# Kernel tuning notes

Measured on AMD Instinct MI355X. Metric: run time of the kernel, lower is better.

The kernel has to match this reference:

```python
import jax, jax.numpy as jnp
import numpy as np

N = 50000      # nodes
E = 600000     # edges
D_IN = 128
D_H = 128
D_OUT = 64


def setup_inputs() -> dict:
    key = jax.random.key(0)
    ks = jax.random.split(key, 10)
    x = jax.random.normal(ks[0], (N, D_IN), dtype=jnp.float32)
    edge_index = jax.random.randint(ks[1], (2, E), 0, N, dtype=jnp.int32)
    def lin(k, fan_out, fan_in):
        s = 1.0 / np.sqrt(fan_in)
        return jax.random.uniform(k, (fan_out, fan_in), jnp.float32, -s, s)
    W0 = lin(ks[2], D_H, D_IN);   b0 = jnp.zeros((D_H,), jnp.float32)
    W1 = lin(ks[3], D_H, D_H);    b1 = jnp.zeros((D_H,), jnp.float32)
    W2 = lin(ks[4], D_H, D_H);    b2 = jnp.zeros((D_H,), jnp.float32)
    W3 = lin(ks[5], D_OUT, D_H);  b3 = jnp.zeros((D_OUT,), jnp.float32)
    return {"x": x, "edge_index": edge_index,
            "W0": W0, "b0": b0, "W1": W1, "b1": b1,
            "W2": W2, "b2": b2, "W3": W3, "b3": b3}


def reference(x, edge_index, W0, b0, W1, b1, W2, b2, W3, b3):
    n = x.shape[0]
    loops = jnp.arange(n, dtype=edge_index.dtype)
    row = jnp.concatenate([edge_index[0], loops])  # sources (with self-loops)
    col = jnp.concatenate([edge_index[1], loops])  # targets
    # symmetric normalization D^-1/2 (A+I) D^-1/2 (PyG GCNConv default)
    deg = jax.ops.segment_sum(jnp.ones(row.shape, x.dtype), col, num_segments=n)
    dinv = jnp.where(deg > 0, jax.lax.rsqrt(deg), 0.0)
    norm = dinv[row] * dinv[col]  # [E+N]

    def gcn_conv(h, W, b):
        h = h @ W.T                              # [n, out]
        msg = h[row] * norm[:, None]             # gather + scale
        out = jax.ops.segment_sum(msg, col, num_segments=n)  # scatter-add
        return out + b

    h = jax.nn.relu(gcn_conv(x, W0, b0))   # Dropout is identity in eval mode
    h = jax.nn.relu(gcn_conv(h, W1, b1))
    h = jax.nn.relu(gcn_conv(h, W2, b2))
    return gcn_conv(h, W3, b3)
```

## Files before the change

kernel.cpp:

```cpp
#include <hip/hip_runtime.h>

#define D_INF 128
#define D_HF  128
#define D_OUTF 64

typedef __attribute__((ext_vector_type(8))) short bf16x8;
typedef __attribute__((ext_vector_type(4))) float f32x4;
typedef unsigned short u16;
typedef unsigned int   u32;

__device__ inline u16 f2bf(float f) {
    u32 u = __float_as_uint(f);
    u32 r = (u + 0x7fffu + ((u >> 16) & 1u)) >> 16;
    return (u16)r;
}
__device__ inline float bf2f(u16 h) { return __uint_as_float(((u32)h) << 16); }

__global__ void k_zero_i32(int* p, int n) {
    int i = blockIdx.x * blockDim.x + threadIdx.x;
    if (i < n) p[i] = 0;
}

__global__ void k_count(const int* __restrict__ colv, int* __restrict__ cnt, int E) {
    int e = blockIdx.x * blockDim.x + threadIdx.x;
    if (e < E) atomicAdd(&cnt[colv[e]], 1);
}

__global__ void k_scan_block(int* __restrict__ cnt, int* __restrict__ rp,
                             int* __restrict__ bsum, float* __restrict__ dinv, int n) {
    __shared__ int sm[256];
    int t = threadIdx.x;
    int i = blockIdx.x * 256 + t;
    int v = (i < n) ? cnt[i] : 0;
    sm[t] = v;
    __syncthreads();
    for (int off = 1; off < 256; off <<= 1) {
        int x = sm[t];
        int y = (t >= off) ? sm[t - off] : 0;
        __syncthreads();
        sm[t] = x + y;
        __syncthreads();
    }
    if (i < n) {
        rp[i] = sm[t] - v;
        dinv[i] = (float)(1.0 / sqrt((double)(v + 1)));
        cnt[i] = 0;
    }
    if (t == 255) bsum[blockIdx.x] = sm[t];
}

__global__ void k_scan_bsum(int* __restrict__ bsum, int nb) {
    __shared__ int sm[256];
    int t = threadIdx.x;
    int v = (t < nb) ? bsum[t] : 0;
    sm[t] = v;
    __syncthreads();
    for (int off = 1; off < 256; off <<= 1) {
        int x = sm[t];
        int y = (t >= off) ? sm[t - off] : 0;
        __syncthreads();
        sm[t] = x + y;
        __syncthreads();
    }
    if (t < nb) bsum[t] = sm[t] - v;
}

__global__ void k_scan_add2(int* __restrict__ rp, const int* __restrict__ bsum, int n) {
    int i = blockIdx.x * 256 + threadIdx.x;
    if (i < n) rp[i] += bsum[blockIdx.x];
}

__global__ void k_scatter(const int* __restrict__ row, const int* __restrict__ colv,
                          const float* __restrict__ dinv, const int* __restrict__ rp,
                          int* __restrict__ fill, int* __restrict__ csr_src,
                          float* __restrict__ csr_w, int E) {
    int e = blockIdx.x * blockDim.x + threadIdx.x;
    if (e >= E) return;
    int r = row[e], c = colv[e];
    int pos = rp[c] + atomicAdd(&fill[c], 1);
    csr_src[pos] = r;
    csr_w[pos] = dinv[r] * dinv[c];
}

__global__ void k_split_x(const float* __restrict__ x, u16* __restrict__ Xcat,
                          int Nreal, int Mpad) {
    int idx = blockIdx.x * 256 + threadIdx.x;
    int total = Mpad * 32;
    if (idx >= total) return;
    const int row = idx >> 5, c4 = (idx & 31) * 4;
    float4 v = make_float4(0.f, 0.f, 0.f, 0.f);
    if (row < Nreal) v = *(const float4*)(x + (size_t)row * 128 + c4);
    u16 h0 = f2bf(v.x), h1 = f2bf(v.y), h2 = f2bf(v.z), h3 = f2bf(v.w);
    u16 l0 = f2bf(v.x - bf2f(h0)), l1 = f2bf(v.y - bf2f(h1));
    u16 l2 = f2bf(v.z - bf2f(h2)), l3 = f2bf(v.w - bf2f(h3));
    u16* dst = Xcat + (size_t)row * 256 + c4;
    *(u32*)(dst)       = (u32)h0 | ((u32)h1 << 16);
    *(u32*)(dst + 2)   = (u32)h2 | ((u32)h3 << 16);
    *(u32*)(dst + 128) = (u32)l0 | ((u32)l1 << 16);
    *(u32*)(dst + 130) = (u32)l2 | ((u32)l3 << 16);
}

__global__ void k_split_w(const float* __restrict__ W0, const float* __restrict__ W1,
                          const float* __restrict__ W2, const float* __restrict__ W3,
                          u16* __restrict__ Wcat) {
    const int l = blockIdx.y;
    const float* W = (l == 0) ? W0 : (l == 1) ? W1 : (l == 2) ? W2 : W3;
    const int rows = (l == 3) ? 64 : 128;
    int idx = blockIdx.x * 256 + threadIdx.x;
    if (idx >= rows * 128) return;
    const int r = idx >> 7, c = idx & 127;
    float v = W[idx];
    u16 h = f2bf(v);
    u16 lo = f2bf(v - bf2f(h));
    u16* dst = Wcat + (size_t)l * 128 * 256 + (size_t)r * 256 + c;
    dst[0]   = h;
    dst[128] = lo;
}

template <int FM>
__global__ __launch_bounds__(256)
void k_gemm_mfma(const u16* __restrict__ Xcat, const u16* __restrict__ Wcat,
                 float* __restrict__ H) {
    constexpr int Dout = (FM == 4) ? 128 : 64;
    const int tid = threadIdx.x;
    const int wave = tid >> 6, lane = tid & 63;
    const int wm = (FM == 4) ? (wave >> 1) : wave;
    const int wn = (FM == 4) ? (wave & 1) : 0;
    const int row_base = blockIdx.x * 128 + wm * (FM * 16);
    const int col_base = wn * 64;
    const int lr = lane & 15;
    const int kg = lane >> 4;

    f32x4 acc[FM][4] = {};

    #pragma unroll 2
    for (int ks = 0; ks < 8; ++ks) {
        const int k0 = ks * 32 + kg * 8;
        bf16x8 a[FM], b[4];
        #pragma unroll
        for (int i = 0; i < FM; ++i)
            a[i] = *(const bf16x8*)(Xcat + (size_t)(row_base + i * 16 + lr) * 256 + k0);
        #pragma unroll
        for (int j = 0; j < 4; ++j)
            b[j] = *(const bf16x8*)(Wcat + (size_t)(col_base + j * 16 + lr) * 256 + k0);
        #pragma unroll
        for (int i = 0; i < FM; ++i)
            #pragma unroll
            for (int j = 0; j < 4; ++j)
                acc[i][j] = __builtin_amdgcn_mfma_f32_16x16x32_bf16(a[i], b[j], acc[i][j], 0, 0, 0);
    }

    #pragma unroll
    for (int i = 0; i < FM; ++i) {
        const int r0 = row_base + i * 16 + kg * 4;
        #pragma unroll
        for (int j = 0; j < 4; ++j) {
            const int c = col_base + j * 16 + lr;
            #pragma unroll
            for (int q = 0; q < 4; ++q)
                H[(size_t)(r0 + q) * Dout + c] = acc[i][j][q];
        }
    }
}

template <int D, int OUT_MODE>
__global__ void k_agg_gather(const float* __restrict__ H, const float* __restrict__ dinv,
                             const int* __restrict__ rp, const int* __restrict__ csr_src,
                             const float* __restrict__ csr_w, const float* __restrict__ b,
                             void* __restrict__ out, int N, int E) {
    const int node = blockIdx.x * 4 + (threadIdx.x >> 6);
    const int lane = threadIdx.x & 63;
    if (node >= N) return;
    const int beg = rp[node];
    const int end = (node == N - 1) ? E : rp[node + 1];
    const int deg = end - beg;
    const float di = dinv[node];
    const double wself = (double)di * (double)di;

    if (D == 128) {
        const int d0 = lane * 2;
        double a0[8] = {}, a1[8] = {};
        {
            const float2 hs = *(const float2*)(H + (size_t)node * D + d0);
            a0[0] = wself * hs.x; a1[0] = wself * hs.y;
        }
        for (int base = 0; base < deg; base += 64) {
            const int m = min(64, deg - base);
            int s_l = 0; float w_l = 0.f;
            if (lane < m) {
                s_l = csr_src[beg + base + lane];
                w_l = csr_w[beg + base + lane];
            }
            const int m16 = (m + 15) & ~15;
            for (int j = 0; j < m16; j += 16) {
                int s[16]; float w[16];
                #pragma unroll
                for (int q = 0; q < 16; ++q) {
                    s[q] = __shfl(s_l, j + q);
                    w[q] = __shfl(w_l, j + q);
                }
                float2 h[16];
                #pragma unroll
                for (int q = 0; q < 16; ++q)
                    h[q] = *(const float2*)(H + (size_t)s[q] * D + d0);
                #pragma unroll
                for (int q = 0; q < 16; ++q) {
                    a0[q & 7] += (double)w[q] * h[q].x;
                    a1[q & 7] += (double)w[q] * h[q].y;
                }
            }
        }
        double A0 = ((a0[0] + a0[1]) + (a0[2] + a0[3])) + ((a0[4] + a0[5]) + (a0[6] + a0[7]));
        double A1 = ((a1[0] + a1[1]) + (a1[2] + a1[3])) + ((a1[4] + a1[5]) + (a1[6] + a1[7]));
        float v0 = (float)(A0 + (double)b[d0]);
        float v1 = (float)(A1 + (double)b[d0 + 1]);
        if (OUT_MODE == 1) {
            v0 = fmaxf(v0, 0.0f); v1 = fmaxf(v1, 0.0f);
            const u16 h0 = f2bf(v0), h1 = f2bf(v1);
            const u16 l0 = f2bf(v0 - bf2f(h0)), l1 = f2bf(v1 - bf2f(h1));
            u16* xc = (u16*)out + (size_t)node * 256 + d0;
            *(u32*)(xc)       = (u32)h0 | ((u32)h1 << 16);
            *(u32*)(xc + 128) = (u32)l0 | ((u32)l1 << 16);
        } else {
            *(float2*)((float*)out + (size_t)node * D + d0) = make_float2(v0, v1);
        }
    } else {
        const int half = lane >> 5;
        const int l32 = lane & 31;
        const int d0 = l32 * 2;
        double a0[8] = {}, a1[8] = {};
        if (half == 0) {
            const float2 hs = *(const float2*)(H + (size_t)node * D + d0);
            a0[0] = wself * hs.x; a1[0] = wself * hs.y;
        }
        for (int base = 0; base < deg; base += 64) {
            const int m = min(64, deg - base);
            int s_l = 0; float w_l = 0.f;
            if (lane < m) {
                s_l = csr_src[beg + base + lane];
                w_l = csr_w[beg + base + lane];
            }
            const int m16 = (m + 15) & ~15;
            for (int j = 0; j < m16; j += 16) {
                int s[8]; float w[8];
                #pragma unroll
                for (int q = 0; q < 8; ++q) {
                    const int e = j + 2 * q + half;
                    s[q] = __shfl(s_l, e);
                    w[q] = __shfl(w_l, e);
                }
                float2 h[8];
                #pragma unroll
                for (int q = 0; q < 8; ++q)
                    h[q] = *(const float2*)(H + (size_t)s[q] * D + d0);
                #pragma unroll
                for (int q = 0; q < 8; ++q) {
                    a0[q] += (double)w[q] * h[q].x;
                    a1[q] += (double)w[q] * h[q].y;
                }
            }
        }
        double A0 = ((a0[0] + a0[1]) + (a0[2] + a0[3])) + ((a0[4] + a0[5]) + (a0[6] + a0[7]));
        double A1 = ((a1[0] + a1[1]) + (a1[2] + a1[3])) + ((a1[4] + a1[5]) + (a1[6] + a1[7]));
        A0 += __shfl_xor(A0, 32);
        A1 += __shfl_xor(A1, 32);
        if (half == 0) {
            float v0 = (float)(A0 + (double)b[d0]);
            float v1 = (float)(A1 + (double)b[d0 + 1]);
            *(float2*)((float*)out + (size_t)node * D + d0) = make_float2(v0, v1);
        }
    }
}

extern "C" void kernel_launch(void* const* d_in, const int* in_sizes, int n_in,
                              void* d_out, int out_size, void* d_ws, size_t ws_size,
                              hipStream_t stream) {
    const float* x  = (const float*)d_in[0];
    const int*   ei = (const int*)d_in[1];
    const float* W[4] = {(const float*)d_in[2], (const float*)d_in[4],
                         (const float*)d_in[6], (const float*)d_in[8]};
    const float* B[4] = {(const float*)d_in[3], (const float*)d_in[5],
                         (const float*)d_in[7], (const float*)d_in[9]};
    const int N = in_sizes[0] / D_INF;
    const int E = in_sizes[1] / 2;
    const int Mpad = (N + 127) & ~127;
    const int* row  = ei;
    const int* colv = ei + E;

    size_t nPad = ((size_t)N + 255) & ~(size_t)255;
    size_t ePad = ((size_t)E + 255) & ~(size_t)255;
    float* dinv    = (float*)d_ws;
    int*   cnt     = (int*)(dinv + nPad);
    int*   bsum    = cnt + nPad;
    int*   rp      = bsum + 256;
    int*   csr_src = rp + nPad;
    float* csr_w   = (float*)(csr_src + ePad);
    float* Hbuf    = csr_w + ePad;
    u16*   Xcat    = (u16*)(Hbuf + (size_t)Mpad * 128);
    u16*   Wcat    = Xcat + (size_t)Mpad * 256;

    const int TB = 256;
    int nbN = (N + TB - 1) / TB;
    int nbE = (E + TB - 1) / TB;

    k_zero_i32<<<nbN, TB, 0, stream>>>(cnt, N);
    k_count<<<nbE, TB, 0, stream>>>(colv, cnt, E);
    k_scan_block<<<nbN, TB, 0, stream>>>(cnt, rp, bsum, dinv, N);
    k_scan_bsum<<<1, 256, 0, stream>>>(bsum, nbN);
    k_scan_add2<<<nbN, TB, 0, stream>>>(rp, bsum, N);
    k_scatter<<<nbE, TB, 0, stream>>>(row, colv, dinv, rp, cnt, csr_src, csr_w, E);

    k_split_x<<<(Mpad * 32 + TB - 1) / TB, TB, 0, stream>>>(x, Xcat, N, Mpad);
    {
        dim3 g(64, 4);
        k_split_w<<<g, TB, 0, stream>>>(W[0], W[1], W[2], W[3], Wcat);
    }

    const int aggGrid = (N + 3) / 4;
    const int gemmGrid = Mpad / 128;

    for (int l = 0; l < 3; ++l) {
        k_gemm_mfma<4><<<gemmGrid, 256, 0, stream>>>(Xcat, Wcat + (size_t)l * 128 * 256, Hbuf);
        k_agg_gather<128, 1><<<aggGrid, TB, 0, stream>>>(Hbuf, dinv, rp, csr_src, csr_w,
                                                         B[l], (void*)Xcat, N, E);
    }
    k_gemm_mfma<2><<<gemmGrid, 256, 0, stream>>>(Xcat, Wcat + (size_t)3 * 128 * 256, Hbuf);
    k_agg_gather<64, 0><<<aggGrid, TB, 0, stream>>>(Hbuf, dinv, rp, csr_src, csr_w,
                                                    B[3], d_out, N, E);
}
```

Baseline: 331.9 us.

## Bucket CSR edges by source-node quartile and gather per phase

Builds the CSR with four sub-buckets per destination node, keyed by which quarter of the node range the source falls in. Each aggregation walks the buckets in order, so the gathers tend to stay within a narrower address range. The edge-batch unroll drops from 16 to 8, which cuts padding waste on low-degree nodes. In exchange, the prefix scan covers four times as many entries, there is an extra degree kernel, and the per-phase loop adds overhead with less memory-level parallelism per batch.

```diff
diff --git a/kernel.cpp b/kernel.cpp
--- a/kernel.cpp
+++ b/kernel.cpp
@@ -3,6 +3,7 @@
 #define D_INF 128
 #define D_HF  128
 #define D_OUTF 64
+#define NPH 4
 
 typedef __attribute__((ext_vector_type(8))) short bf16x8;
 typedef __attribute__((ext_vector_type(4))) float f32x4;
@@ -21,13 +22,23 @@
     if (i < n) p[i] = 0;
 }
 
-__global__ void k_count(const int* __restrict__ colv, int* __restrict__ cnt, int E) {
+__global__ void k_count4(const int* __restrict__ rowv, const int* __restrict__ colv,
+                         int* __restrict__ cnt4, int E, int q4) {
     int e = blockIdx.x * blockDim.x + threadIdx.x;
-    if (e < E) atomicAdd(&cnt[colv[e]], 1);
+    if (e >= E) return;
+    int ph = min(NPH - 1, rowv[e] / q4);
+    atomicAdd(&cnt4[colv[e] * NPH + ph], 1);
+}
+
+__global__ void k_dinv4(const int* __restrict__ cnt4, float* __restrict__ dinv, int n) {
+    int i = blockIdx.x * blockDim.x + threadIdx.x;
+    if (i >= n) return;
+    int deg = cnt4[i * NPH] + cnt4[i * NPH + 1] + cnt4[i * NPH + 2] + cnt4[i * NPH + 3] + 1;
+    dinv[i] = (float)(1.0 / sqrt((double)deg));
 }
 
 __global__ void k_scan_block(int* __restrict__ cnt, int* __restrict__ rp,
-                             int* __restrict__ bsum, float* __restrict__ dinv, int n) {
+                             int* __restrict__ bsum, int n) {
     __shared__ int sm[256];
     int t = threadIdx.x;
     int i = blockIdx.x * 256 + t;
@@ -43,19 +54,18 @@
     }
     if (i < n) {
         rp[i] = sm[t] - v;
-        dinv[i] = (float)(1.0 / sqrt((double)(v + 1)));
         cnt[i] = 0;
     }
     if (t == 255) bsum[blockIdx.x] = sm[t];
 }
 
 __global__ void k_scan_bsum(int* __restrict__ bsum, int nb) {
-    __shared__ int sm[256];
+    __shared__ int sm[1024];
     int t = threadIdx.x;
     int v = (t < nb) ? bsum[t] : 0;
     sm[t] = v;
     __syncthreads();
-    for (int off = 1; off < 256; off <<= 1) {
+    for (int off = 1; off < 1024; off <<= 1) {
         int x = sm[t];
         int y = (t >= off) ? sm[t - off] : 0;
         __syncthreads();
@@ -70,14 +80,16 @@
     if (i < n) rp[i] += bsum[blockIdx.x];
 }
 
-__global__ void k_scatter(const int* __restrict__ row, const int* __restrict__ colv,
-                          const float* __restrict__ dinv, const int* __restrict__ rp,
+__global__ void k_scatter(const int* __restrict__ rowv, const int* __restrict__ colv,
+                          const float* __restrict__ dinv, const int* __restrict__ rpp,
                           int* __restrict__ fill, int* __restrict__ csr_src,
-                          float* __restrict__ csr_w, int E) {
+                          float* __restrict__ csr_w, int E, int q4) {
     int e = blockIdx.x * blockDim.x + threadIdx.x;
     if (e >= E) return;
-    int r = row[e], c = colv[e];
-    int pos = rp[c] + atomicAdd(&fill[c], 1);
+    int r = rowv[e], c = colv[e];
+    int ph = min(NPH - 1, r / q4);
+    int slot = c * NPH + ph;
+    int pos = rpp[slot] + atomicAdd(&fill[slot], 1);
     csr_src[pos] = r;
     csr_w[pos] = dinv[r] * dinv[c];
 }
@@ -165,17 +177,15 @@
 
 template <int D, int OUT_MODE>
 __global__ void k_agg_gather(const float* __restrict__ H, const float* __restrict__ dinv,
-                             const int* __restrict__ rp, const int* __restrict__ csr_src,
+                             const int* __restrict__ rpp, const int* __restrict__ csr_src,
                              const float* __restrict__ csr_w, const float* __restrict__ b,
                              void* __restrict__ out, int N, int E) {
     const int node = blockIdx.x * 4 + (threadIdx.x >> 6);
     const int lane = threadIdx.x & 63;
     if (node >= N) return;
-    const int beg = rp[node];
-    const int end = (node == N - 1) ? E : rp[node + 1];
-    const int deg = end - beg;
     const float di = dinv[node];
     const double wself = (double)di * (double)di;
+    const int* rpn = rpp + NPH * node;
 
     if (D == 128) {
         const int d0 = lane * 2;
@@ -184,29 +194,35 @@
             const float2 hs = *(const float2*)(H + (size_t)node * D + d0);
             a0[0] = wself * hs.x; a1[0] = wself * hs.y;
         }
-        for (int base = 0; base < deg; base += 64) {
-            const int m = min(64, deg - base);
-            int s_l = 0; float w_l = 0.f;
-            if (lane < m) {
-                s_l = csr_src[beg + base + lane];
-                w_l = csr_w[beg + base + lane];
-            }
-            const int m16 = (m + 15) & ~15;
-            for (int j = 0; j < m16; j += 16) {
-                int s[16]; float w[16];
-                #pragma unroll
-                for (int q = 0; q < 16; ++q) {
-                    s[q] = __shfl(s_l, j + q);
-                    w[q] = __shfl(w_l, j + q);
+        #pragma unroll
+        for (int ph = 0; ph < NPH; ++ph) {
+            const int pbeg = rpn[ph];
+            const int pend = (node == N - 1 && ph == NPH - 1) ? E : rpn[ph + 1];
+            const int pdeg = pend - pbeg;
+            for (int base = 0; base < pdeg; base += 64) {
+                const int m = min(64, pdeg - base);
+                int s_l = 0; float w_l = 0.f;
+                if (lane < m) {
+                    s_l = csr_src[pbeg + base + lane];
+                    w_l = csr_w[pbeg + base + lane];
                 }
-                float2 h[16];
-                #pragma unroll
-                for (int q = 0; q < 16; ++q)
-                    h[q] = *(const float2*)(H + (size_t)s[q] * D + d0);
-                #pragma unroll
-                for (int q = 0; q < 16; ++q) {
-                    a0[q & 7] += (double)w[q] * h[q].x;
-                    a1[q & 7] += (double)w[q] * h[q].y;
+                const int m8 = (m + 7) & ~7;
+                for (int j = 0; j < m8; j += 8) {
+                    int s[8]; float w[8];
+                    #pragma unroll
+                    for (int q = 0; q < 8; ++q) {
+                        s[q] = __shfl(s_l, j + q);
+                        w[q] = __shfl(w_l, j + q);
+                    }
+                    float2 h[8];
+                    #pragma unroll
+                    for (int q = 0; q < 8; ++q)
+                        h[q] = *(const float2*)(H + (size_t)s[q] * D + d0);
+                    #pragma unroll
+                    for (int q = 0; q < 8; ++q) {
+                        a0[q] += (double)w[q] * h[q].x;
+                        a1[q] += (double)w[q] * h[q].y;
+                    }
                 }
             }
         }
@@ -228,40 +244,46 @@
         const int half = lane >> 5;
         const int l32 = lane & 31;
         const int d0 = l32 * 2;
-        double a0[8] = {}, a1[8] = {};
+        double a0[4] = {}, a1[4] = {};
         if (half == 0) {
             const float2 hs = *(const float2*)(H + (size_t)node * D + d0);
             a0[0] = wself * hs.x; a1[0] = wself * hs.y;
         }
-        for (int base = 0; base < deg; base += 64) {
-            const int m = min(64, deg - base);
-            int s_l = 0; float w_l = 0.f;
-            if (lane < m) {
-                s_l = csr_src[beg + base + lane];
-                w_l = csr_w[beg + base + lane];
-            }
-            const int m16 = (m + 15) & ~15;
-            for (int j = 0; j < m16; j += 16) {
-                int s[8]; float w[8];
-                #pragma unroll
-                for (int q = 0; q < 8; ++q) {
-                    const int e = j + 2 * q + half;
-                    s[q] = __shfl(s_l, e);
-                    w[q] = __shfl(w_l, e);
+        #pragma unroll
+        for (int ph = 0; ph < NPH; ++ph) {
+            const int pbeg = rpn[ph];
+            const int pend = (node == N - 1 && ph == NPH - 1) ? E : rpn[ph + 1];
+            const int pdeg = pend - pbeg;
+            for (int base = 0; base < pdeg; base += 64) {
+                const int m = min(64, pdeg - base);
+                int s_l = 0; float w_l = 0.f;
+                if (lane < m) {
+                    s_l = csr_src[pbeg + base + lane];
+                    w_l = csr_w[pbeg + base + lane];
                 }
-                float2 h[8];
-                #pragma unroll
-                for (int q = 0; q < 8; ++q)
-                    h[q] = *(const float2*)(H + (size_t)s[q] * D + d0);
-                #pragma unroll
-                for (int q = 0; q < 8; ++q) {
-                    a0[q] += (double)w[q] * h[q].x;
-                    a1[q] += (double)w[q] * h[q].y;
+                const int m8 = (m + 7) & ~7;
+                for (int j = 0; j < m8; j += 8) {
+                    int s[4]; float w[4];
+                    #pragma unroll
+                    for (int q = 0; q < 4; ++q) {
+                        const int e = j + 2 * q + half;
+                        s[q] = __shfl(s_l, e);
+                        w[q] = __shfl(w_l, e);
+                    }
+                    float2 h[4];
+                    #pragma unroll
+                    for (int q = 0; q < 4; ++q)
+                        h[q] = *(const float2*)(H + (size_t)s[q] * D + d0);
+                    #pragma unroll
+                    for (int q = 0; q < 4; ++q) {
+                        a0[q] += (double)w[q] * h[q].x;
+                        a1[q] += (double)w[q] * h[q].y;
+                    }
                 }
             }
         }
-        double A0 = ((a0[0] + a0[1]) + (a0[2] + a0[3])) + ((a0[4] + a0[5]) + (a0[6] + a0[7]));
-        double A1 = ((a1[0] + a1[1]) + (a1[2] + a1[3])) + ((a1[4] + a1[5]) + (a1[6] + a1[7]));
+        double A0 = (a0[0] + a0[1]) + (a0[2] + a0[3]);
+        double A1 = (a1[0] + a1[1]) + (a1[2] + a1[3]);
         A0 += __shfl_xor(A0, 32);
         A1 += __shfl_xor(A1, 32);
         if (half == 0) {
@@ -284,31 +306,36 @@
     const int N = in_sizes[0] / D_INF;
     const int E = in_sizes[1] / 2;
     const int Mpad = (N + 127) & ~127;
-    const int* row  = ei;
+    const int* rowv = ei;
     const int* colv = ei + E;
-
-    size_t nPad = ((size_t)N + 255) & ~(size_t)255;
-    size_t ePad = ((size_t)E + 255) & ~(size_t)255;
+    const int N4 = N * NPH;
+    const int q4 = (N + NPH - 1) / NPH;
+
+    size_t nPad  = ((size_t)N + 255) & ~(size_t)255;
+    size_t n4Pad = ((size_t)N4 + 255) & ~(size_t)255;
+    size_t ePad  = ((size_t)E + 255) & ~(size_t)255;
     float* dinv    = (float*)d_ws;
-    int*   cnt     = (int*)(dinv + nPad);
-    int*   bsum    = cnt + nPad;
-    int*   rp      = bsum + 256;
-    int*   csr_src = rp + nPad;
+    int*   cnt4    = (int*)(dinv + nPad);
+    int*   bsum    = cnt4 + n4Pad;
+    int*   rpp     = bsum + 1024;
+    int*   csr_src = rpp + n4Pad;
     float* csr_w   = (float*)(csr_src + ePad);
     float* Hbuf    = csr_w + ePad;
     u16*   Xcat    = (u16*)(Hbuf + (size_t)Mpad * 128);
     u16*   Wcat    = Xcat + (size_t)Mpad * 256;
 
     const int TB = 256;
-    int nbN = (N + TB - 1) / TB;
-    int nbE = (E + TB - 1) / TB;
-
-    k_zero_i32<<<nbN, TB, 0, stream>>>(cnt, N);
-    k_count<<<nbE, TB, 0, stream>>>(colv, cnt, E);
-    k_scan_block<<<nbN, TB, 0, stream>>>(cnt, rp, bsum, dinv, N);
-    k_scan_bsum<<<1, 256, 0, stream>>>(bsum, nbN);
-    k_scan_add2<<<nbN, TB, 0, stream>>>(rp, bsum, N);
-    k_scatter<<<nbE, TB, 0, stream>>>(row, colv, dinv, rp, cnt, csr_src, csr_w, E);
+    int nbN  = (N + TB - 1) / TB;
+    int nbN4 = (N4 + TB - 1) / TB;
+    int nbE  = (E + TB - 1) / TB;
+
+    k_zero_i32<<<nbN4, TB, 0, stream>>>(cnt4, N4);
+    k_count4<<<nbE, TB, 0, stream>>>(rowv, colv, cnt4, E, q4);
+    k_dinv4<<<nbN, TB, 0, stream>>>(cnt4, dinv, N);
+    k_scan_block<<<nbN4, TB, 0, stream>>>(cnt4, rpp, bsum, N4);
+    k_scan_bsum<<<1, 1024, 0, stream>>>(bsum, nbN4);
+    k_scan_add2<<<nbN4, TB, 0, stream>>>(rpp, bsum, N4);
+    k_scatter<<<nbE, TB, 0, stream>>>(rowv, colv, dinv, rpp, cnt4, csr_src, csr_w, E, q4);
 
     k_split_x<<<(Mpad * 32 + TB - 1) / TB, TB, 0, stream>>>(x, Xcat, N, Mpad);
     {
@@ -321,10 +348,10 @@
 
     for (int l = 0; l < 3; ++l) {
         k_gemm_mfma<4><<<gemmGrid, 256, 0, stream>>>(Xcat, Wcat + (size_t)l * 128 * 256, Hbuf);
-        k_agg_gather<128, 1><<<aggGrid, TB, 0, stream>>>(Hbuf, dinv, rp, csr_src, csr_w,
+        k_agg_gather<128, 1><<<aggGrid, TB, 0, stream>>>(Hbuf, dinv, rpp, csr_src, csr_w,
                                                          B[l], (void*)Xcat, N, E);
     }
     k_gemm_mfma<2><<<gemmGrid, 256, 0, stream>>>(Xcat, Wcat + (size_t)3 * 128 * 256, Hbuf);
-    k_agg_gather<64, 0><<<aggGrid, TB, 0, stream>>>(Hbuf, dinv, rp, csr_src, csr_w,
+    k_agg_gather<64, 0><<<aggGrid, TB, 0, stream>>>(Hbuf, dinv, rpp, csr_src, csr_w,
                                                     B[3], d_out, N, E);
 }
```

After: 420.8 us. +26.8%, slower.
